# Optimization experiments

Hardware: AMD Instinct MI355X
Metric: run time of the kernel (lower is better)

Reference implementation:

```python
import jax, jax.numpy as jnp
import numpy as np

B, HW, N, C, F, ITERS = 32, 4096, 16, 128, 512, 3
EPS_LN = 1e-5
EPS_ATTN = 1e-5


def _ln(x, g, b):
    m = x.mean(-1, keepdims=True)
    v = ((x - m) ** 2).mean(-1, keepdims=True)
    return (x - m) / jnp.sqrt(v + EPS_LN) * g + b


def _gru(x, h, wih, whh, bih, bhh):
    # torch.nn.GRUCell math
    gi = x @ wih.T + bih
    gh = h @ whh.T + bhh
    i_r, i_z, i_n = jnp.split(gi, 3, axis=-1)
    h_r, h_z, h_n = jnp.split(gh, 3, axis=-1)
    r = jax.nn.sigmoid(i_r + h_r)
    z = jax.nn.sigmoid(i_z + h_z)
    n = jnp.tanh(i_n + r * h_n)
    return (1.0 - z) * n + z * h


def setup_inputs() -> dict:
    key = jax.random.key(0)
    ks = jax.random.split(key, 16)
    s = 0.02
    d = {
        'inp': jax.random.normal(ks[0], (B, HW, C), jnp.float32),
        'query': jax.random.normal(ks[1], (B, N, C), jnp.float32),
        'ln_kv_g': jnp.ones((C,), jnp.float32),
        'ln_kv_b': jnp.zeros((C,), jnp.float32),
        'Wk': jax.random.normal(ks[2], (C, C), jnp.float32) * s,
        'Wv': jax.random.normal(ks[3], (C, C), jnp.float32) * s,
        'ln_q_g': jnp.ones((C,), jnp.float32),
        'ln_q_b': jnp.zeros((C,), jnp.float32),
        'Wq': jax.random.normal(ks[4], (C, C), jnp.float32) * s,
        'gru_wih': jax.random.normal(ks[5], (3 * C, C), jnp.float32) * s,
        'gru_whh': jax.random.normal(ks[6], (3 * C, C), jnp.float32) * s,
        'gru_bih': jnp.zeros((3 * C,), jnp.float32),
        'gru_bhh': jnp.zeros((3 * C,), jnp.float32),
        'ln2_g': jnp.ones((C,), jnp.float32),
        'ln2_b': jnp.zeros((C,), jnp.float32),
        'ffn_w1': jax.random.normal(ks[7], (F, C), jnp.float32) * s,
        'ffn_b1': jnp.zeros((F,), jnp.float32),
        'ffn_w2': jax.random.normal(ks[8], (C, F), jnp.float32) * s,
        'ffn_b2': jnp.zeros((C,), jnp.float32),
    }
    return d


def reference(inp, query, ln_kv_g, ln_kv_b, Wk, Wv, ln_q_g, ln_q_b, Wq,
              gru_wih, gru_whh, gru_bih, gru_bhh, ln2_g, ln2_b,
              ffn_w1, ffn_b1, ffn_w2, ffn_b2):
    b, n, c = query.shape
    kv = _ln(inp, ln_kv_g, ln_kv_b)
    k = kv @ Wk.T  # (b, hw, c)
    v = kv @ Wv.T  # (b, hw, c)
    scale = c ** -0.5
    q = query
    a0 = None
    for _ in range(ITERS):
        x = q
        qn = _ln(q, ln_q_g, ln_q_b) @ Wq.T
        logit = jnp.einsum('bqc,bkc->bqk', qn * scale, k)  # (b, n, hw)
        a0 = jax.nn.softmax(logit, axis=1)  # inverted: softmax over slots
        a = a0 / (a0.sum(2, keepdims=True) + EPS_ATTN)  # renorm over keys
        u = jnp.einsum('bqk,bkc->bqc', a, v)
        y = _gru(u.reshape(b * n, c), x.reshape(b * n, c),
                 gru_wih, gru_whh, gru_bih, gru_bhh).reshape(b, n, c)
        z = _ln(y, ln2_g, ln2_b)
        ffn = jax.nn.relu(z @ ffn_w1.T + ffn_b1) @ ffn_w2.T + ffn_b2
        q = y + ffn
    return (q, a0)
```

## Files before the change

### kernel.cpp

```cpp
#include <hip/hip_runtime.h>
#include <math.h>

#define B_ 32
#define HW_ 4096
#define N_ 16
#define C_ 128
#define F_ 512
#define ITERS_ 3
#define EPS_LN 1e-5f
#define EPS_ATTN 1e-5f

typedef __attribute__((ext_vector_type(8))) short short8;
typedef __attribute__((ext_vector_type(4))) float f32x4;

static __device__ __forceinline__ unsigned short f2b(float f) {
    union { float f; unsigned u; } v; v.f = f;
    unsigned r = v.u + 0x7fffu + ((v.u >> 16) & 1u);
    return (unsigned short)(r >> 16);
}
static __device__ __forceinline__ float blo(unsigned u) {
    union { unsigned u; float f; } v; v.u = u << 16; return v.f;
}
static __device__ __forceinline__ float bhi(unsigned u) {
    union { unsigned u; float f; } v; v.u = u & 0xffff0000u; return v.f;
}

__global__ __launch_bounds__(256) void k_prep(
    const float* __restrict__ Wk, const float* __restrict__ Wv,
    const float* __restrict__ wih, const float* __restrict__ whh,
    const float* __restrict__ w1, const float* __restrict__ w2,
    unsigned short* __restrict__ Wk_bf, unsigned short* __restrict__ Wv_bf,
    unsigned short* __restrict__ wih_bf, unsigned short* __restrict__ whh_bf,
    unsigned short* __restrict__ w1_bf, unsigned short* __restrict__ w2_bf,
    const float* __restrict__ query, const float* __restrict__ lnqg,
    const float* __restrict__ lnqb, const float* __restrict__ Wq,
    unsigned short* __restrict__ qn_g)
{
    __shared__ __align__(16) float xq[16 * 128];
    int tid = threadIdx.x;
    if (blockIdx.x < 256) {
        int t = blockIdx.x * 256 + tid;
        const float* src; unsigned short* dst; int off;
        if (t < 4096)       { src = Wk;  dst = Wk_bf;  off = t; }
        else if (t < 8192)  { src = Wv;  dst = Wv_bf;  off = t - 4096; }
        else if (t < 20480) { src = wih; dst = wih_bf; off = t - 8192; }
        else if (t < 32768) { src = whh; dst = whh_bf; off = t - 20480; }
        else if (t < 49152) { src = w1;  dst = w1_bf;  off = t - 32768; }
        else                { src = w2;  dst = w2_bf;  off = t - 49152; }
        float4 a = ((const float4*)src)[off];
        uint2 p;
        p.x = (unsigned)f2b(a.x) | ((unsigned)f2b(a.y) << 16);
        p.y = (unsigned)f2b(a.z) | ((unsigned)f2b(a.w) << 16);
        *(uint2*)(dst + off * 4) = p;
        return;
    }
    int b = blockIdx.x - 256;
    int n = tid >> 4, part = tid & 15;
    int row = b * 16 + n;
    const float4* x4 = (const float4*)(query + row * 128 + part * 8);
    float4 x0 = x4[0], x1 = x4[1];
    float s = x0.x + x0.y + x0.z + x0.w + x1.x + x1.y + x1.z + x1.w;
    float ss = x0.x * x0.x + x0.y * x0.y + x0.z * x0.z + x0.w * x0.w +
               x1.x * x1.x + x1.y * x1.y + x1.z * x1.z + x1.w * x1.w;
    s += __shfl_xor(s, 1); s += __shfl_xor(s, 2); s += __shfl_xor(s, 4); s += __shfl_xor(s, 8);
    ss += __shfl_xor(ss, 1); ss += __shfl_xor(ss, 2); ss += __shfl_xor(ss, 4); ss += __shfl_xor(ss, 8);
    float mean = s * (1.f / 128.f);
    float var = ss * (1.f / 128.f) - mean * mean;
    float rstd = rsqrtf(var + EPS_LN);
    const float4* g4 = (const float4*)(lnqg + part * 8);
    const float4* b4 = (const float4*)(lnqb + part * 8);
    float4 g0 = g4[0], g1 = g4[1], bb0 = b4[0], bb1 = b4[1];
    float4 o0, o1;
    o0.x = (x0.x - mean) * rstd * g0.x + bb0.x;
    o0.y = (x0.y - mean) * rstd * g0.y + bb0.y;
    o0.z = (x0.z - mean) * rstd * g0.z + bb0.z;
    o0.w = (x0.w - mean) * rstd * g0.w + bb0.w;
    o1.x = (x1.x - mean) * rstd * g1.x + bb1.x;
    o1.y = (x1.y - mean) * rstd * g1.y + bb1.y;
    o1.z = (x1.z - mean) * rstd * g1.z + bb1.z;
    o1.w = (x1.w - mean) * rstd * g1.w + bb1.w;
    float4* xrow = (float4*)&xq[n * 128];
    xrow[part * 2] = o0;
    xrow[part * 2 + 1] = o1;
    __syncthreads();
    float o[8] = {0.f, 0.f, 0.f, 0.f, 0.f, 0.f, 0.f, 0.f};
    const float4* xv4 = (const float4*)&xq[n * 128];
#pragma unroll 4
    for (int j = 0; j < 32; j++) {
        float4 xv = xv4[j];
#pragma unroll
        for (int i = 0; i < 8; i++) {
            float4 w = ((const float4*)(Wq + (part * 8 + i) * 128))[j];
            o[i] += w.x * xv.x + w.y * xv.y + w.z * xv.z + w.w * xv.w;
        }
    }
    const float scale = 0.08838834764831845f;
#pragma unroll
    for (int i = 0; i < 8; i++)
        qn_g[row * 128 + part * 8 + i] = f2b(o[i] * scale);
}

__global__ __launch_bounds__(256) void k_kvproj(
    const float* __restrict__ inp, const float* __restrict__ lng,
    const float* __restrict__ lnb, const unsigned short* __restrict__ Wk_bf,
    const unsigned short* __restrict__ Wv_bf, unsigned short* __restrict__ Kbf,
    unsigned short* __restrict__ Vt)
{
    __shared__ __align__(16) unsigned short W_lds[128 * 128];
    __shared__ __align__(16) unsigned short T_lds[8960];
    const int tid = threadIdx.x;
    const int wave = tid >> 6, lane = tid & 63;
    const int l15 = lane & 15, q4 = lane >> 4;
    const int kof = q4 * 8;
    const int tile0 = blockIdx.x * 64;
    const int b = tile0 >> 12;
    const int hwbase = tile0 & (HW_ - 1);

    const int srow = tid >> 1, shalf = tid & 1;
    const int sswz = srow & 7;

    float x[4][8];
    {
        const float* rowp = inp + (tile0 + (wave << 4) + l15) * C_;
        float s = 0.f, ss = 0.f;
#pragma unroll
        for (int ks = 0; ks < 4; ks++) {
#pragma unroll
            for (int h = 0; h < 2; h++) {
                float4 v = *(const float4*)(rowp + ks * 32 + kof + h * 4);
                x[ks][h * 4 + 0] = v.x; x[ks][h * 4 + 1] = v.y;
                x[ks][h * 4 + 2] = v.z; x[ks][h * 4 + 3] = v.w;
                s += v.x + v.y + v.z + v.w;
                ss += v.x * v.x + v.y * v.y + v.z * v.z + v.w * v.w;
            }
        }
        s += __shfl_xor(s, 16);  s += __shfl_xor(s, 32);
        ss += __shfl_xor(ss, 16); ss += __shfl_xor(ss, 32);
        float mean = s * (1.f / 128.f);
        float var = ss * (1.f / 128.f) - mean * mean;
        float rstd = rsqrtf(var + EPS_LN);
#pragma unroll
        for (int ks = 0; ks < 4; ks++) {
#pragma unroll
            for (int h = 0; h < 2; h++) {
                float4 g = *(const float4*)(lng + ks * 32 + kof + h * 4);
                float4 bb = *(const float4*)(lnb + ks * 32 + kof + h * 4);
                x[ks][h * 4 + 0] = (x[ks][h * 4 + 0] - mean) * rstd * g.x + bb.x;
                x[ks][h * 4 + 1] = (x[ks][h * 4 + 1] - mean) * rstd * g.y + bb.y;
                x[ks][h * 4 + 2] = (x[ks][h * 4 + 2] - mean) * rstd * g.z + bb.z;
                x[ks][h * 4 + 3] = (x[ks][h * 4 + 3] - mean) * rstd * g.w + bb.w;
            }
        }
    }
    short8 af[4];
#pragma unroll
    for (int ks = 0; ks < 4; ks++) {
        union { short8 s8; unsigned u[4]; } p;
#pragma unroll
        for (int j = 0; j < 4; j++)
            p.u[j] = (unsigned)f2b(x[ks][2 * j]) | ((unsigned)f2b(x[ks][2 * j + 1]) << 16);
        af[ks] = p.s8;
    }

    {
        const uint4* gW = (const uint4*)Wk_bf;
#pragma unroll
        for (int j = 0; j < 8; j++) {
            int c = shalf * 8 + j;
            uint4 w = gW[srow * 16 + c];
            *(uint4*)&W_lds[srow * 128 + (c ^ sswz) * 8] = w;
        }
    }
    __syncthreads();

    f32x4 acc[8];
#pragma unroll
    for (int nt = 0; nt < 8; nt++) {
        acc[nt] = (f32x4){0.f, 0.f, 0.f, 0.f};
#pragma unroll
        for (int ks = 0; ks < 4; ks++) {
            short8 bf = *(const short8*)&W_lds[(nt * 16 + l15) * 128 + ((ks * 4 + q4) ^ (l15 & 7)) * 8];
            acc[nt] = __builtin_amdgcn_mfma_f32_16x16x32_bf16(af[ks], bf, acc[nt], 0, 0, 0);
        }
    }
#pragma unroll
    for (int nt = 0; nt < 8; nt++) {
        int c = nt * 16 + l15;
#pragma unroll
        for (int i = 0; i < 4; i++)
            T_lds[((wave << 4) + (q4 << 2) + i) * 132 + c] = f2b(acc[nt][i]);
    }
    __syncthreads();
    {
        int row = tid >> 2, part = tid & 3;
        uint4* dst = (uint4*)&Kbf[(b * HW_ + hwbase + row) * C_ + part * 32];
#pragma unroll
        for (int j = 0; j < 4; j++)
            dst[j] = *(const uint4*)&T_lds[row * 132 + part * 32 + j * 8];
    }
    {
        const uint4* gW = (const uint4*)Wv_bf;
#pragma unroll
        for (int j = 0; j < 8; j++) {
            int c = shalf * 8 + j;
            uint4 w = gW[srow * 16 + c];
            *(uint4*)&W_lds[srow * 128 + (c ^ sswz) * 8] = w;
        }
    }
    __syncthreads();
#pragma unroll
    for (int nt = 0; nt < 8; nt++) {
        acc[nt] = (f32x4){0.f, 0.f, 0.f, 0.f};
#pragma unroll
        for (int ks = 0; ks < 4; ks++) {
            short8 bf = *(const short8*)&W_lds[(nt * 16 + l15) * 128 + ((ks * 4 + q4) ^ (l15 & 7)) * 8];
            acc[nt] = __builtin_amdgcn_mfma_f32_16x16x32_bf16(af[ks], bf, acc[nt], 0, 0, 0);
        }
    }
    __syncthreads();
#pragma unroll
    for (int nt = 0; nt < 8; nt++) {
        int c = nt * 16 + l15;
#pragma unroll
        for (int i = 0; i < 4; i++)
            T_lds[c * 70 + (wave << 4) + (q4 << 2) + i] = f2b(acc[nt][i]);
    }
    __syncthreads();
    {
        int c = tid >> 1, half = tid & 1;
        uint4* dst = (uint4*)&Vt[(b * C_ + c) * HW_ + hwbase + half * 32];
#pragma unroll
        for (int j = 0; j < 4; j++)
            dst[j] = *(const uint4*)&T_lds[c * 70 + half * 32 + j * 8];
    }
}

__global__ __launch_bounds__(128) void k_attn(
    const unsigned short* __restrict__ qn_g, const unsigned short* __restrict__ Kbf,
    const unsigned short* __restrict__ Vt, float* __restrict__ Upart,
    float* __restrict__ rspart, float* __restrict__ a0_out, int last)
{
    __shared__ __align__(16) float Ul[2][16 * 132];
    __shared__ __align__(16) unsigned short Pb[2][16 * 72];
    __shared__ float rsw[2][16];
    const int b = blockIdx.y, chunk = blockIdx.x;
    const int tid = threadIdx.x;
    const int wave = tid >> 6, lane = tid & 63;
    const int l15 = lane & 15, q4 = lane >> 4;
    const int kof = q4 * 8;
    const int hwb = chunk * 128 + wave * 64;

    short8 aq[4];
#pragma unroll
    for (int ks = 0; ks < 4; ks++)
        aq[ks] = *(const short8*)&qn_g[(b * 16 + l15) * 128 + ks * 32 + kof];
    short8 av[8][2];
#pragma unroll
    for (int ct = 0; ct < 8; ct++) {
#pragma unroll
        for (int k2 = 0; k2 < 2; k2++)
            av[ct][k2] = *(const short8*)&Vt[(b * C_ + ct * 16 + l15) * HW_ + hwb + k2 * 32 + kof];
    }

    unsigned short* Pw = &Pb[wave][0];
    float rs[4] = {0.f, 0.f, 0.f, 0.f};
#pragma unroll
    for (int s = 0; s < 4; s++) {
        int hwt = hwb + s * 16;
        f32x4 sa = {0.f, 0.f, 0.f, 0.f};
#pragma unroll
        for (int ks = 0; ks < 4; ks++) {
            short8 bk = *(const short8*)&Kbf[(b * HW_ + hwt + l15) * C_ + ks * 32 + kof];
            sa = __builtin_amdgcn_mfma_f32_16x16x32_bf16(aq[ks], bk, sa, 0, 0, 0);
        }
        float mx = fmaxf(fmaxf(sa[0], sa[1]), fmaxf(sa[2], sa[3]));
        mx = fmaxf(mx, __shfl_xor(mx, 16));
        mx = fmaxf(mx, __shfl_xor(mx, 32));
        float e[4]; float ssum = 0.f;
#pragma unroll
        for (int i = 0; i < 4; i++) { e[i] = __expf(sa[i] - mx); ssum += e[i]; }
        ssum += __shfl_xor(ssum, 16);
        ssum += __shfl_xor(ssum, 32);
        float inv = 1.f / ssum;
#pragma unroll
        for (int i = 0; i < 4; i++) {
            float a0v = e[i] * inv;
            rs[i] += a0v;
            if (last) a0_out[(b * 16 + q4 * 4 + i) * HW_ + hwt + l15] = a0v;
            Pw[(q4 * 4 + i) * 72 + s * 16 + l15] = f2b(a0v);
        }
    }
#pragma unroll
    for (int i = 0; i < 4; i++) {
        rs[i] += __shfl_xor(rs[i], 1);
        rs[i] += __shfl_xor(rs[i], 2);
        rs[i] += __shfl_xor(rs[i], 4);
        rs[i] += __shfl_xor(rs[i], 8);
    }
    if (l15 == 0) {
#pragma unroll
        for (int i = 0; i < 4; i++) rsw[wave][q4 * 4 + i] = rs[i];
    }
    short8 bp0 = *(const short8*)&Pw[l15 * 72 + kof];
    short8 bp1 = *(const short8*)&Pw[l15 * 72 + 32 + kof];
#pragma unroll
    for (int ct = 0; ct < 8; ct++) {
        f32x4 ua = __builtin_amdgcn_mfma_f32_16x16x32_bf16(av[ct][0], bp0, (f32x4){0.f, 0.f, 0.f, 0.f}, 0, 0, 0);
        ua = __builtin_amdgcn_mfma_f32_16x16x32_bf16(av[ct][1], bp1, ua, 0, 0, 0);
        *(f32x4*)&Ul[wave][l15 * 132 + ct * 16 + (q4 << 2)] = ua;
    }
    __syncthreads();
    {
        float* up = Upart + (b * 32 + chunk) * 2048;
#pragma unroll
        for (int k = 0; k < 16; k++) {
            int idx = tid + k * 128;
            int q = idx >> 7, c = idx & 127;
            up[idx] = Ul[0][q * 132 + c] + Ul[1][q * 132 + c];
        }
        if (tid < 16)
            rspart[(b * 32 + chunk) * 16 + tid] = rsw[0][tid] + rsw[1][tid];
    }
}

__global__ __launch_bounds__(256) void k_tail(
    const float* __restrict__ Upart, const float* __restrict__ rspart,
    const float* __restrict__ hsrc, float* __restrict__ q_buf,
    const unsigned short* __restrict__ wih_bf, const unsigned short* __restrict__ whh_bf,
    const float* __restrict__ bih, const float* __restrict__ bhh,
    const float* __restrict__ ln2g, const float* __restrict__ ln2b,
    const unsigned short* __restrict__ w1_bf, const float* __restrict__ b1,
    const unsigned short* __restrict__ w2_bf, const float* __restrict__ b2,
    const float* __restrict__ lnqg, const float* __restrict__ lnqb,
    const float* __restrict__ Wq, unsigned short* __restrict__ qn_g,
    float* __restrict__ out_q, int last)
{
    __shared__ __align__(16) float u_l[128];
    __shared__ __align__(16) float h_l[128];
    __shared__ __align__(16) float g_l[768];
    __shared__ __align__(16) float z_l[128];
    __shared__ __align__(16) float y_l[128];
    __shared__ __align__(16) float h1_l[512];
    __shared__ __align__(16) float red[256];
    __shared__ float stats[2];
    __shared__ float srs;
    const int tid = threadIdx.x;
    const int row = blockIdx.x;
    const int b = row >> 4, q = row & 15;
    const int lane = tid & 63;

    {
        int c = tid & 127, h = tid >> 7;
        float part = 0.f;
#pragma unroll
        for (int ch = 0; ch < 16; ch++)
            part += Upart[(b * 32 + h * 16 + ch) * 2048 + q * 128 + c];
        red[tid] = part;
        if (tid < 128) h_l[tid] = hsrc[row * 128 + tid];
        if (tid < 64) {
            float v = (lane < 32) ? rspart[(b * 32 + lane) * 16 + q] : 0.f;
#pragma unroll
            for (int off = 1; off < 64; off <<= 1) v += __shfl_xor(v, off);
            if (tid == 0) srs = v;
        }
    }
    __syncthreads();
    if (tid < 128)
        u_l[tid] = (red[tid] + red[tid + 128]) / (srs + EPS_ATTN);
    __syncthreads();
#pragma unroll
    for (int o3 = 0; o3 < 3; o3++) {
        int o = tid + o3 * 256;
        const unsigned short* wrow;
        const float* src;
        float bias;
        if (o < 384) { wrow = wih_bf + o * 128; src = u_l; bias = bih[o]; }
        else         { wrow = whh_bf + (o - 384) * 128; src = h_l; bias = bhh[o - 384]; }
        const uint4* w4 = (const uint4*)wrow;
        const float4* s4 = (const float4*)src;
        float acc = 0.f;
#pragma unroll 8
        for (int j = 0; j < 16; j++) {
            uint4 w = w4[j];
            float4 aA = s4[2 * j], aB = s4[2 * j + 1];
            acc += blo(w.x) * aA.x + bhi(w.x) * aA.y + blo(w.y) * aA.z + bhi(w.y) * aA.w
                 + blo(w.z) * aB.x + bhi(w.z) * aB.y + blo(w.w) * aB.z + bhi(w.w) * aB.w;
        }
        g_l[o] = acc + bias;
    }
    __syncthreads();
    if (tid < 128) {
        int c = tid;
        float ir = g_l[c], iz = g_l[128 + c], in_ = g_l[256 + c];
        float hr = g_l[384 + c], hz = g_l[512 + c], hn = g_l[640 + c];
        float rr = 1.f / (1.f + expf(-(ir + hr)));
        float zz = 1.f / (1.f + expf(-(iz + hz)));
        float nn = tanhf(in_ + rr * hn);
        y_l[c] = (1.f - zz) * nn + zz * h_l[c];
    }
    __syncthreads();
    if (tid < 64) {
        float v0 = y_l[lane], v1 = y_l[lane + 64];
        float s = v0 + v1, ss = v0 * v0 + v1 * v1;
#pragma unroll
        for (int off = 1; off < 64; off <<= 1) {
            s += __shfl_xor(s, off);
            ss += __shfl_xor(ss, off);
        }
        if (tid == 0) {
            float mean = s * (1.f / 128.f);
            float var = ss * (1.f / 128.f) - mean * mean;
            stats[0] = mean;
            stats[1] = rsqrtf(var + EPS_LN);
        }
    }
    __syncthreads();
    if (tid < 128)
        z_l[tid] = (y_l[tid] - stats[0]) * stats[1] * ln2g[tid] + ln2b[tid];
    __syncthreads();
#pragma unroll
    for (int f2i = 0; f2i < 2; f2i++) {
        int f = tid + f2i * 256;
        const uint4* w4 = (const uint4*)(w1_bf + f * 128);
        const float4* s4 = (const float4*)z_l;
        float acc = 0.f;
#pragma unroll 8
        for (int j = 0; j < 16; j++) {
            uint4 w = w4[j];
            float4 aA = s4[2 * j], aB = s4[2 * j + 1];
            acc += blo(w.x) * aA.x + bhi(w.x) * aA.y + blo(w.y) * aA.z + bhi(w.y) * aA.w
                 + blo(w.z) * aB.x + bhi(w.z) * aB.y + blo(w.w) * aB.z + bhi(w.w) * aB.w;
        }
        h1_l[f] = fmaxf(acc + b1[f], 0.f);
    }
    __syncthreads();
    {
        int c = tid & 127, h = tid >> 7;
        const uint4* w4 = (const uint4*)(w2_bf + c * 512 + h * 256);
        const float4* hh = (const float4*)&h1_l[h * 256];
        float acc = 0.f;
#pragma unroll 8
        for (int j = 0; j < 32; j++) {
            uint4 w = w4[j];
            float4 hA = hh[2 * j], hB = hh[2 * j + 1];
            acc += blo(w.x) * hA.x + bhi(w.x) * hA.y + blo(w.y) * hA.z + bhi(w.y) * hA.w
                 + blo(w.z) * hB.x + bhi(w.z) * hB.y + blo(w.w) * hB.z + bhi(w.w) * hB.w;
        }
        red[tid] = acc;
    }
    __syncthreads();
    float q_new = 0.f;
    if (tid < 128) {
        q_new = y_l[tid] + red[tid] + red[tid + 128] + b2[tid];
        q_buf[row * 128 + tid] = q_new;
        if (last) out_q[row * 128 + tid] = q_new;
    }
    if (!last) {
        __syncthreads();
        if (tid < 128) y_l[tid] = q_new;
        __syncthreads();
        if (tid < 64) {
            float v0 = y_l[lane], v1 = y_l[lane + 64];
            float s = v0 + v1, ss = v0 * v0 + v1 * v1;
#pragma unroll
            for (int off = 1; off < 64; off <<= 1) {
                s += __shfl_xor(s, off);
                ss += __shfl_xor(ss, off);
            }
            if (tid == 0) {
                float mean = s * (1.f / 128.f);
                float var = ss * (1.f / 128.f) - mean * mean;
                stats[0] = mean;
                stats[1] = rsqrtf(var + EPS_LN);
            }
        }
        __syncthreads();
        if (tid < 128)
            z_l[tid] = (y_l[tid] - stats[0]) * stats[1] * lnqg[tid] + lnqb[tid];
        __syncthreads();
        {
            int c = tid & 127, h = tid >> 7;
            const float4* w4 = (const float4*)(Wq + c * 128 + h * 64);
            const float4* zz = (const float4*)&z_l[h * 64];
            float acc = 0.f;
#pragma unroll 8
            for (int j = 0; j < 16; j++) {
                float4 w = w4[j], v = zz[j];
                acc += w.x * v.x + w.y * v.y + w.z * v.z + w.w * v.w;
            }
            red[tid] = acc;
        }
        __syncthreads();
        if (tid < 128)
            qn_g[row * 128 + tid] = f2b((red[tid] + red[tid + 128]) * 0.08838834764831845f);
    }
}

extern "C" void kernel_launch(void* const* d_in, const int* in_sizes, int n_in,
                              void* d_out, int out_size, void* d_ws, size_t ws_size,
                              hipStream_t stream) {
    const float* inp     = (const float*)d_in[0];
    const float* query   = (const float*)d_in[1];
    const float* ln_kv_g = (const float*)d_in[2];
    const float* ln_kv_b = (const float*)d_in[3];
    const float* Wk      = (const float*)d_in[4];
    const float* Wv      = (const float*)d_in[5];
    const float* ln_q_g  = (const float*)d_in[6];
    const float* ln_q_b  = (const float*)d_in[7];
    const float* Wq      = (const float*)d_in[8];
    const float* gru_wih = (const float*)d_in[9];
    const float* gru_whh = (const float*)d_in[10];
    const float* gru_bih = (const float*)d_in[11];
    const float* gru_bhh = (const float*)d_in[12];
    const float* ln2_g   = (const float*)d_in[13];
    const float* ln2_b   = (const float*)d_in[14];
    const float* ffn_w1  = (const float*)d_in[15];
    const float* ffn_b1  = (const float*)d_in[16];
    const float* ffn_w2  = (const float*)d_in[17];
    const float* ffn_b2  = (const float*)d_in[18];

    char* ws = (char*)d_ws;
    unsigned short* Kbf    = (unsigned short*)ws;
    unsigned short* Vt     = (unsigned short*)(ws + 33554432);
    float* q_buf           = (float*)(ws + 67108864);
    float* Upart           = (float*)(ws + 67371008);
    float* rspart          = (float*)(ws + 75759616);
    unsigned short* qn_g   = (unsigned short*)(ws + 75825152);
    unsigned short* Wk_bf  = (unsigned short*)(ws + 75956224);
    unsigned short* Wv_bf  = (unsigned short*)(ws + 75988992);
    unsigned short* wih_bf = (unsigned short*)(ws + 76021760);
    unsigned short* whh_bf = (unsigned short*)(ws + 76120064);
    unsigned short* w1_bf  = (unsigned short*)(ws + 76218368);
    unsigned short* w2_bf  = (unsigned short*)(ws + 76349440);

    float* out_q  = (float*)d_out;
    float* out_a0 = out_q + B_ * N_ * C_;

    k_prep<<<dim3(288), dim3(256), 0, stream>>>(
        Wk, Wv, gru_wih, gru_whh, ffn_w1, ffn_w2,
        Wk_bf, Wv_bf, wih_bf, whh_bf, w1_bf, w2_bf,
        query, ln_q_g, ln_q_b, Wq, qn_g);
    k_kvproj<<<dim3((B_ * HW_) / 64), dim3(256), 0, stream>>>(
        inp, ln_kv_g, ln_kv_b, Wk_bf, Wv_bf, Kbf, Vt);

    for (int it = 0; it < ITERS_; it++) {
        int last = (it == ITERS_ - 1) ? 1 : 0;
        const float* hsrc = (it == 0) ? query : q_buf;
        k_attn<<<dim3(32, B_), dim3(128), 0, stream>>>(
            qn_g, Kbf, Vt, Upart, rspart, out_a0, last);
        k_tail<<<dim3(B_ * N_), dim3(256), 0, stream>>>(
            Upart, rspart, hsrc, q_buf, wih_bf, whh_bf, gru_bih, gru_bhh,
            ln2_g, ln2_b, w1_bf, ffn_b1, w2_bf, ffn_b2,
            ln_q_g, ln_q_b, Wq, qn_g, out_q, last);
    }
}
```

Baseline: 330.0 us.

## Read K/V weights directly from global in kvproj; split attn over 4 waves

In the KV projection kernel, the Wk/Wv tiles are no longer staged into a 32 KB LDS buffer. MFMA B-fragments are read straight from global memory, which removes two block barriers and frees LDS for more resident blocks. The cost is redundant global/L2 reads of the weights by every wave. Separately, the attention kernel now runs 4 waves of 32 keys each instead of 2 waves of 64, which raises parallelism per block and cuts register pressure, at the cost of a wider cross-wave reduction in LDS.

```diff
diff --git a/kernel.cpp b/kernel.cpp
--- a/kernel.cpp
+++ b/kernel.cpp
@@ -106,7 +106,6 @@
     const unsigned short* __restrict__ Wv_bf, unsigned short* __restrict__ Kbf,
     unsigned short* __restrict__ Vt)
 {
-    __shared__ __align__(16) unsigned short W_lds[128 * 128];
     __shared__ __align__(16) unsigned short T_lds[8960];
     const int tid = threadIdx.x;
     const int wave = tid >> 6, lane = tid & 63;
@@ -116,9 +115,6 @@
     const int b = tile0 >> 12;
     const int hwbase = tile0 & (HW_ - 1);
 
-    const int srow = tid >> 1, shalf = tid & 1;
-    const int sswz = srow & 7;
-
     float x[4][8];
     {
         const float* rowp = inp + (tile0 + (wave << 4) + l15) * C_;
@@ -162,24 +158,13 @@
         af[ks] = p.s8;
     }
 
-    {
-        const uint4* gW = (const uint4*)Wk_bf;
-#pragma unroll
-        for (int j = 0; j < 8; j++) {
-            int c = shalf * 8 + j;
-            uint4 w = gW[srow * 16 + c];
-            *(uint4*)&W_lds[srow * 128 + (c ^ sswz) * 8] = w;
-        }
-    }
-    __syncthreads();
-
     f32x4 acc[8];
 #pragma unroll
     for (int nt = 0; nt < 8; nt++) {
         acc[nt] = (f32x4){0.f, 0.f, 0.f, 0.f};
 #pragma unroll
         for (int ks = 0; ks < 4; ks++) {
-            short8 bf = *(const short8*)&W_lds[(nt * 16 + l15) * 128 + ((ks * 4 + q4) ^ (l15 & 7)) * 8];
+            short8 bf = *(const short8*)&Wk_bf[(nt * 16 + l15) * 128 + ks * 32 + kof];
             acc[nt] = __builtin_amdgcn_mfma_f32_16x16x32_bf16(af[ks], bf, acc[nt], 0, 0, 0);
         }
     }
@@ -198,23 +183,14 @@
         for (int j = 0; j < 4; j++)
             dst[j] = *(const uint4*)&T_lds[row * 132 + part * 32 + j * 8];
     }
-    {
-        const uint4* gW = (const uint4*)Wv_bf;
-#pragma unroll
-        for (int j = 0; j < 8; j++) {
-            int c = shalf * 8 + j;
-            uint4 w = gW[srow * 16 + c];
-            *(uint4*)&W_lds[srow * 128 + (c ^ sswz) * 8] = w;
-        }
-    }
-    __syncthreads();
+    f32x4 acc2[8];
 #pragma unroll
     for (int nt = 0; nt < 8; nt++) {
-        acc[nt] = (f32x4){0.f, 0.f, 0.f, 0.f};
+        acc2[nt] = (f32x4){0.f, 0.f, 0.f, 0.f};
 #pragma unroll
         for (int ks = 0; ks < 4; ks++) {
-            short8 bf = *(const short8*)&W_lds[(nt * 16 + l15) * 128 + ((ks * 4 + q4) ^ (l15 & 7)) * 8];
-            acc[nt] = __builtin_amdgcn_mfma_f32_16x16x32_bf16(af[ks], bf, acc[nt], 0, 0, 0);
+            short8 bf = *(const short8*)&Wv_bf[(nt * 16 + l15) * 128 + ks * 32 + kof];
+            acc2[nt] = __builtin_amdgcn_mfma_f32_16x16x32_bf16(af[ks], bf, acc2[nt], 0, 0, 0);
         }
     }
     __syncthreads();
@@ -223,7 +199,7 @@
         int c = nt * 16 + l15;
 #pragma unroll
         for (int i = 0; i < 4; i++)
-            T_lds[c * 70 + (wave << 4) + (q4 << 2) + i] = f2b(acc[nt][i]);
+            T_lds[c * 70 + (wave << 4) + (q4 << 2) + i] = f2b(acc2[nt][i]);
     }
     __syncthreads();
     {
@@ -235,37 +211,34 @@
     }
 }
 
-__global__ __launch_bounds__(128) void k_attn(
+__global__ __launch_bounds__(256) void k_attn(
     const unsigned short* __restrict__ qn_g, const unsigned short* __restrict__ Kbf,
     const unsigned short* __restrict__ Vt, float* __restrict__ Upart,
     float* __restrict__ rspart, float* __restrict__ a0_out, int last)
 {
-    __shared__ __align__(16) float Ul[2][16 * 132];
-    __shared__ __align__(16) unsigned short Pb[2][16 * 72];
-    __shared__ float rsw[2][16];
+    __shared__ __align__(16) float Ul[4][16 * 132];
+    __shared__ __align__(16) unsigned short Pb[4][16 * 40];
+    __shared__ float rsw[4][16];
     const int b = blockIdx.y, chunk = blockIdx.x;
     const int tid = threadIdx.x;
     const int wave = tid >> 6, lane = tid & 63;
     const int l15 = lane & 15, q4 = lane >> 4;
     const int kof = q4 * 8;
-    const int hwb = chunk * 128 + wave * 64;
+    const int hwb = chunk * 128 + wave * 32;
 
     short8 aq[4];
 #pragma unroll
     for (int ks = 0; ks < 4; ks++)
         aq[ks] = *(const short8*)&qn_g[(b * 16 + l15) * 128 + ks * 32 + kof];
-    short8 av[8][2];
-#pragma unroll
-    for (int ct = 0; ct < 8; ct++) {
-#pragma unroll
-        for (int k2 = 0; k2 < 2; k2++)
-            av[ct][k2] = *(const short8*)&Vt[(b * C_ + ct * 16 + l15) * HW_ + hwb + k2 * 32 + kof];
-    }
+    short8 av[8];
+#pragma unroll
+    for (int ct = 0; ct < 8; ct++)
+        av[ct] = *(const short8*)&Vt[(b * C_ + ct * 16 + l15) * HW_ + hwb + kof];
 
     unsigned short* Pw = &Pb[wave][0];
     float rs[4] = {0.f, 0.f, 0.f, 0.f};
 #pragma unroll
-    for (int s = 0; s < 4; s++) {
+    for (int s = 0; s < 2; s++) {
         int hwt = hwb + s * 16;
         f32x4 sa = {0.f, 0.f, 0.f, 0.f};
 #pragma unroll
@@ -287,7 +260,7 @@
             float a0v = e[i] * inv;
             rs[i] += a0v;
             if (last) a0_out[(b * 16 + q4 * 4 + i) * HW_ + hwt + l15] = a0v;
-            Pw[(q4 * 4 + i) * 72 + s * 16 + l15] = f2b(a0v);
+            Pw[(q4 * 4 + i) * 40 + s * 16 + l15] = f2b(a0v);
         }
     }
 #pragma unroll
@@ -301,25 +274,25 @@
 #pragma unroll
         for (int i = 0; i < 4; i++) rsw[wave][q4 * 4 + i] = rs[i];
     }
-    short8 bp0 = *(const short8*)&Pw[l15 * 72 + kof];
-    short8 bp1 = *(const short8*)&Pw[l15 * 72 + 32 + kof];
+    short8 bp = *(const short8*)&Pw[l15 * 40 + kof];
 #pragma unroll
     for (int ct = 0; ct < 8; ct++) {
-        f32x4 ua = __builtin_amdgcn_mfma_f32_16x16x32_bf16(av[ct][0], bp0, (f32x4){0.f, 0.f, 0.f, 0.f}, 0, 0, 0);
-        ua = __builtin_amdgcn_mfma_f32_16x16x32_bf16(av[ct][1], bp1, ua, 0, 0, 0);
+        f32x4 ua = __builtin_amdgcn_mfma_f32_16x16x32_bf16(av[ct], bp, (f32x4){0.f, 0.f, 0.f, 0.f}, 0, 0, 0);
         *(f32x4*)&Ul[wave][l15 * 132 + ct * 16 + (q4 << 2)] = ua;
     }
     __syncthreads();
     {
         float* up = Upart + (b * 32 + chunk) * 2048;
 #pragma unroll
-        for (int k = 0; k < 16; k++) {
-            int idx = tid + k * 128;
+        for (int k = 0; k < 8; k++) {
+            int idx = tid + k * 256;
             int q = idx >> 7, c = idx & 127;
-            up[idx] = Ul[0][q * 132 + c] + Ul[1][q * 132 + c];
+            up[idx] = Ul[0][q * 132 + c] + Ul[1][q * 132 + c] +
+                      Ul[2][q * 132 + c] + Ul[3][q * 132 + c];
         }
         if (tid < 16)
-            rspart[(b * 32 + chunk) * 16 + tid] = rsw[0][tid] + rsw[1][tid];
+            rspart[(b * 32 + chunk) * 16 + tid] =
+                rsw[0][tid] + rsw[1][tid] + rsw[2][tid] + rsw[3][tid];
     }
 }
 
@@ -546,7 +519,7 @@
     for (int it = 0; it < ITERS_; it++) {
         int last = (it == ITERS_ - 1) ? 1 : 0;
         const float* hsrc = (it == 0) ? query : q_buf;
-        k_attn<<<dim3(32, B_), dim3(128), 0, stream>>>(
+        k_attn<<<dim3(32, B_), dim3(256), 0, stream>>>(
             qn_g, Kbf, Vt, Upart, rspart, out_a0, last);
         k_tail<<<dim3(B_ * N_), dim3(256), 0, stream>>>(
             Upart, rspart, hsrc, q_buf, wih_bf, whh_bf, gru_bih, gru_bhh,
```

Measured after the change: 370.6 us. 12.3% more time.
